# Performance work log

Measured on AMD Instinct MI355X. Metric: run time of the kernel, lower is better.

Reference implementation:

```python
import jax, jax.numpy as jnp
import numpy as np
import math

B, N, C = 16, 4096, 256
WS = 8            # window_size
NH = 8            # num_heads
HD = C // NH      # head_dim = 32
LK = 32           # linformer compressed length
G = 16            # global bank tokens


def setup_inputs() -> dict:
    key = jax.random.key(0)
    ks = jax.random.split(key, 10)
    x = jax.random.normal(ks[0], (B, N, C), dtype=jnp.float32)
    W_qkv = jax.random.normal(ks[1], (C, 3 * C), dtype=jnp.float32) * 0.02
    b_qkv = jnp.zeros((3 * C,), dtype=jnp.float32)
    E_k = jax.random.normal(ks[2], (WS * WS, LK), dtype=jnp.float32) * 0.02
    E_v = jax.random.normal(ks[3], (WS * WS, LK), dtype=jnp.float32) * 0.02
    k_bank = jax.random.normal(ks[4], (G, C), dtype=jnp.float32)
    v_bank = jax.random.normal(ks[5], (G, C), dtype=jnp.float32)
    W_proj = jax.random.normal(ks[6], (C, C), dtype=jnp.float32) * 0.02
    b_proj = jnp.zeros((C,), dtype=jnp.float32)
    return {"x": x, "W_qkv": W_qkv, "b_qkv": b_qkv, "E_k": E_k, "E_v": E_v,
            "k_bank": k_bank, "v_bank": v_bank, "W_proj": W_proj, "b_proj": b_proj,
            "window_size": WS, "num_heads": NH}


def reference(x, W_qkv, b_qkv, E_k, E_v, k_bank, v_bank, W_proj, b_proj, window_size, num_heads):
    Bb, Nn, Cc = x.shape
    Hs = int(math.isqrt(Nn))          # H = W = sqrt(N), divisible by window_size here
    ws = window_size
    nh = Hs // ws                      # windows per side
    hd = Cc // num_heads
    NW = ws * ws                       # tokens per window

    # ---- window partition: [B,N,C] -> [BW, NW, C]
    xw = x.reshape(Bb, nh, ws, nh, ws, Cc).transpose(0, 1, 3, 2, 4, 5)
    xw = xw.reshape(Bb * nh * nh, NW, Cc)
    BW = xw.shape[0]

    # ---- qkv projection and head split: (3, BW, H, NW, hd)
    qkv = (xw @ W_qkv + b_qkv).reshape(BW, NW, 3, num_heads, hd)
    qkv = qkv.transpose(2, 0, 3, 1, 4)
    q, k, v = qkv[0], qkv[1], qkv[2]

    # ---- Linformer KV compression: NW == seq_len (no pad branch)
    k_c = jnp.einsum('nk,bhnd->bhkd', E_k, k)   # [BW,H,LK,hd]
    v_c = jnp.einsum('nk,bhnd->bhkd', E_v, v)

    # ---- global memory bank, broadcast to all windows: [BW,H,G,hd]
    Gt = k_bank.shape[0]
    kb = jnp.broadcast_to(k_bank.reshape(Gt, num_heads, hd).transpose(1, 0, 2)[None],
                          (BW, num_heads, Gt, hd))
    vb = jnp.broadcast_to(v_bank.reshape(Gt, num_heads, hd).transpose(1, 0, 2)[None],
                          (BW, num_heads, Gt, hd))

    k_full = jnp.concatenate([k_c, kb], axis=2)  # [BW,H,LK+G,hd]
    v_full = jnp.concatenate([v_c, vb], axis=2)

    # ---- SDPA (dropout_p = 0)
    scale = 1.0 / math.sqrt(hd)
    scores = jnp.einsum('bhqd,bhkd->bhqk', q, k_full) * scale
    attn = jax.nn.softmax(scores, axis=-1)
    out = jnp.einsum('bhqk,bhkd->bhqd', attn, v_full)     # [BW,H,NW,hd]

    out = out.transpose(0, 2, 1, 3).reshape(BW, NW, Cc)
    out = out @ W_proj + b_proj

    # ---- window reverse: [BW,NW,C] -> [B,N,C]
    out = out.reshape(Bb, nh, nh, ws, ws, Cc).transpose(0, 1, 3, 2, 4, 5)
    out = out.reshape(Bb, Hs * Hs, Cc)
    return out
```

## Files before the change

kernel.cpp:

```cpp
#include <hip/hip_runtime.h>
#include <hip/hip_bf16.h>


typedef unsigned int uint;
typedef __attribute__((ext_vector_type(8))) short short8;
typedef __attribute__((ext_vector_type(4))) float f32x4;
typedef __attribute__((ext_vector_type(4))) uint uintx4;

__device__ __forceinline__ float bup(uint hs) {
    return __uint_as_float(hs << 16);
}
__device__ __forceinline__ uint f2b(float f) {
    __hip_bfloat16 h = __float2bfloat16(f);
    unsigned short u;
    __builtin_memcpy(&u, &h, 2);
    return (uint)u;
}
__device__ __forceinline__ uint f2b2(float a, float b) {
    __hip_bfloat162 h = __float22bfloat162_rn(make_float2(a, b));
    uint u;
    __builtin_memcpy(&u, &h, 4);
    return u;
}
__device__ __forceinline__ f32x4 mfma16(short8 a, short8 b, f32x4 c) {
    return __builtin_amdgcn_mfma_f32_16x16x32_bf16(a, b, c, 0, 0, 0);
}
__device__ __forceinline__ int sw256(int r, int c) { return r * 256 + (c ^ ((r & 7) << 3)); }

__device__ __forceinline__ short8 xpose(f32x4 a, f32x4 b, float s, int lane) {
    const uint pa0 = f2b2(a[0] * s, a[1] * s), pa1 = f2b2(a[2] * s, a[3] * s);
    const uint pb0 = f2b2(b[0] * s, b[1] * s), pb1 = f2b2(b[2] * s, b[3] * s);
    const int s0 = ((lane >> 4) & 1) * 32 + (lane & 15);
    const int s1 = s0 + 16;
    const uint w0a = __shfl(pa0, s0), w0b = __shfl(pb0, s0);
    const uint w1a = __shfl(pa1, s0), w1b = __shfl(pb1, s0);
    const uint w2a = __shfl(pa0, s1), w2b = __shfl(pb0, s1);
    const uint w3a = __shfl(pa1, s1), w3b = __shfl(pb1, s1);
    const bool hi = lane >= 32;
    uintx4 u;
    u[0] = hi ? w0b : w0a;
    u[1] = hi ? w1b : w1a;
    u[2] = hi ? w2b : w2a;
    u[3] = hi ? w3b : w3a;
    short8 r;
    __builtin_memcpy(&r, &u, 16);
    return r;
}
__device__ __forceinline__ short8 xpose_half(f32x4 a, float s, int lane) {
    const uint pa0 = f2b2(a[0] * s, a[1] * s), pa1 = f2b2(a[2] * s, a[3] * s);
    const int s0 = ((lane >> 4) & 1) * 32 + (lane & 15);
    const int s1 = s0 + 16;
    const uint w0a = __shfl(pa0, s0);
    const uint w1a = __shfl(pa1, s0);
    const uint w2a = __shfl(pa0, s1);
    const uint w3a = __shfl(pa1, s1);
    const bool hi = lane >= 32;
    uintx4 u;
    u[0] = hi ? 0u : w0a;
    u[1] = hi ? 0u : w1a;
    u[2] = hi ? 0u : w2a;
    u[3] = hi ? 0u : w3a;
    short8 r;
    __builtin_memcpy(&r, &u, 16);
    return r;
}

#define WS_WHQ 0
#define WS_WHP 196608
#define WS_WLP 262144
#define WS_EKT 327680
#define WS_EVT 329728
#define WS_KBF 331776
#define WS_VBF 335872

__global__ void __launch_bounds__(256)
eswa_prep(const float* __restrict__ Wqkv, const float* __restrict__ Wproj,
          const float* __restrict__ Ek, const float* __restrict__ Ev,
          const float* __restrict__ kbank, const float* __restrict__ vbank,
          short* __restrict__ wsp)
{
    const int blk = blockIdx.x, thr = threadIdx.x;
    if (blk < 192) {
        const int jh = blk & 1;
        const int g = (blk >> 1) * 256 + thr;
        const int lane = g & 63, tk = (g >> 6) & 7, tn = g >> 9;
        const int quad = lane >> 4, l16 = lane & 15;
        const int c = tn * 16 + l16;
        const int r0 = tk * 32 + quad * 8 + jh * 4;
        const float w0 = Wqkv[(r0 + 0) * 768 + c], w1 = Wqkv[(r0 + 1) * 768 + c];
        const float w2 = Wqkv[(r0 + 2) * 768 + c], w3 = Wqkv[(r0 + 3) * 768 + c];
        *(uint2*)(wsp + WS_WHQ + ((tn * 8 + tk) * 64 + lane) * 8 + jh * 4) =
            make_uint2(f2b2(w0, w1), f2b2(w2, w3));
    } else if (blk < 256) {
        const int idx = blk - 192, jh = idx & 1;
        const int g = (idx >> 1) * 256 + thr;
        const int lane = g & 63, tk = (g >> 6) & 7, tn = g >> 9;
        const int quad = lane >> 4, l16 = lane & 15;
        const int c = tn * 16 + l16;
        const int r0 = tk * 32 + quad * 8 + jh * 4;
        float w[4];
        #pragma unroll
        for (int j = 0; j < 4; ++j) w[j] = Wproj[(r0 + j) * 256 + c];
        const uint h01 = f2b2(w[0], w[1]), h23 = f2b2(w[2], w[3]);
        const float l0 = w[0] - bup(h01 & 0xffffu), l1 = w[1] - bup(h01 >> 16);
        const float l2 = w[2] - bup(h23 & 0xffffu), l3 = w[3] - bup(h23 >> 16);
        const int o = ((tn * 8 + tk) * 64 + lane) * 8 + jh * 4;
        *(uint2*)(wsp + WS_WHP + o) = make_uint2(h01, h23);
        *(uint2*)(wsp + WS_WLP + o) = make_uint2(f2b2(l0, l1), f2b2(l2, l3));
    } else if (blk < 258) {
        const float* E = (blk == 256) ? Ek : Ev;
        const int base = (blk == 256) ? WS_EKT : WS_EVT;
        const int lane = thr & 63, tk = (thr >> 6) & 1, tm = (thr >> 7) & 1;
        const int quad = lane >> 4, l16 = lane & 15;
        const int lk = tm * 16 + l16;
        uint pk[4];
        #pragma unroll
        for (int jp = 0; jp < 4; ++jp) {
            const int t = tk * 32 + quad * 8 + jp * 2;
            pk[jp] = f2b2(E[t * 32 + lk], E[(t + 1) * 32 + lk]);
        }
        *(uint4*)(wsp + base + ((tm * 2 + tk) * 64 + lane) * 8) =
            make_uint4(pk[0], pk[1], pk[2], pk[3]);
    } else {
        for (int idx = thr; idx < 512; idx += 256) {
            const int hh = idx >> 6, l = idx & 63;
            const int l16 = l & 15, q = l >> 4;
            uint pk[4];
            #pragma unroll
            for (int jp = 0; jp < 4; ++jp)
                pk[jp] = f2b2(kbank[l16 * 256 + hh * 32 + q * 8 + jp * 2],
                              kbank[l16 * 256 + hh * 32 + q * 8 + jp * 2 + 1]);
            *(uint4*)(wsp + WS_KBF + idx * 8) = make_uint4(pk[0], pk[1], pk[2], pk[3]);
        }
        for (int idx = thr; idx < 1024; idx += 256) {
            const int hh = idx >> 7, md = (idx >> 6) & 1, l = idx & 63;
            const int l16 = l & 15, q = l >> 4;
            uint pk[4] = {0u, 0u, 0u, 0u};
            if (q < 2) {
                #pragma unroll
                for (int jp = 0; jp < 4; ++jp)
                    pk[jp] = f2b2(vbank[(q * 8 + jp * 2) * 256 + hh * 32 + md * 16 + l16],
                                  vbank[(q * 8 + jp * 2 + 1) * 256 + hh * 32 + md * 16 + l16]);
            }
            *(uint4*)(wsp + WS_VBF + idx * 8) = make_uint4(pk[0], pk[1], pk[2], pk[3]);
        }
    }
}

#define SMEM_BYTES 32768

__global__ void __launch_bounds__(512, 3)
eswa_main(const float* __restrict__ x, const float* __restrict__ bqkv,
          const float* __restrict__ bproj, const short* __restrict__ wsp,
          float* __restrict__ out)
{
    extern __shared__ char smem[];
    short* xh   = (short*)smem;
    short* attn = (short*)smem;

    const int tid  = threadIdx.x;
    const int wave = tid >> 6;
    const int lane = tid & 63;
    const int quad = lane >> 4;
    const int l16  = lane & 15;
    const int h    = wave;

    const int b  = blockIdx.x >> 6;
    const int w  = blockIdx.x & 63;
    const int rw = w >> 3;
    const int cw = w & 7;

    #pragma unroll
    for (int i = 0; i < 8; ++i) {
        const int vi = tid + 512 * i;
        const int t  = vi >> 6;
        const int c  = (vi & 63) * 4;
        const int n  = (rw * 8 + (t >> 3)) * 64 + cw * 8 + (t & 7);
        const float4 xv = *(const float4*)(x + (size_t)(b * 4096 + n) * 256 + c);
        *(uint2*)(xh + sw256(t, c)) = make_uint2(f2b2(xv.x, xv.y), f2b2(xv.z, xv.w));
    }
    __syncthreads();

    const short* WF = wsp + WS_WHQ;

    short8 kcf[2], vcf[2];
    {
        f32x4 acc[2][4];
        #pragma unroll
        for (int nd = 0; nd < 2; ++nd) {
            const float bk = bqkv[256 + h * 32 + nd * 16 + l16];
            #pragma unroll
            for (int mt = 0; mt < 4; ++mt) acc[nd][mt] = (f32x4){bk, bk, bk, bk};
        }
        #pragma unroll 2
        for (int tk = 0; tk < 8; ++tk) {
            short8 xf[4];
            #pragma unroll
            for (int mt = 0; mt < 4; ++mt)
                xf[mt] = *(const short8*)(xh + sw256(mt * 16 + l16, tk * 32 + quad * 8));
            #pragma unroll
            for (int nd = 0; nd < 2; ++nd) {
                const short8 wf =
                    *(const short8*)(WF + (((16 + h * 2 + nd) * 8 + tk) * 64 + lane) * 8);
                #pragma unroll
                for (int mt = 0; mt < 4; ++mt) acc[nd][mt] = mfma16(xf[mt], wf, acc[nd][mt]);
            }
        }
        short8 kfr[2][2];
        #pragma unroll
        for (int nd = 0; nd < 2; ++nd)
            #pragma unroll
            for (int kk = 0; kk < 2; ++kk)
                kfr[nd][kk] = xpose(acc[nd][2 * kk], acc[nd][2 * kk + 1], 1.0f, lane);
        short8 ekf[2][2];
        #pragma unroll
        for (int tm = 0; tm < 2; ++tm)
            #pragma unroll
            for (int kk = 0; kk < 2; ++kk)
                ekf[tm][kk] = *(const short8*)(wsp + WS_EKT + ((tm * 2 + kk) * 64 + lane) * 8);
        f32x4 ck[2][2];
        #pragma unroll
        for (int md = 0; md < 2; ++md)
            #pragma unroll
            for (int nl = 0; nl < 2; ++nl) ck[md][nl] = (f32x4){0, 0, 0, 0};
        #pragma unroll
        for (int kk = 0; kk < 2; ++kk)
            #pragma unroll
            for (int md = 0; md < 2; ++md)
                #pragma unroll
                for (int nl = 0; nl < 2; ++nl)
                    ck[md][nl] = mfma16(kfr[md][kk], ekf[nl][kk], ck[md][nl]);
        #pragma unroll
        for (int nl = 0; nl < 2; ++nl)
            kcf[nl] = xpose(ck[0][nl], ck[1][nl], 1.0f, lane);
    }
    {
        f32x4 acc[2][4];
        #pragma unroll
        for (int nd = 0; nd < 2; ++nd) {
            const float bv = bqkv[512 + h * 32 + nd * 16 + l16];
            #pragma unroll
            for (int mt = 0; mt < 4; ++mt) acc[nd][mt] = (f32x4){bv, bv, bv, bv};
        }
        #pragma unroll 2
        for (int tk = 0; tk < 8; ++tk) {
            short8 xf[4];
            #pragma unroll
            for (int mt = 0; mt < 4; ++mt)
                xf[mt] = *(const short8*)(xh + sw256(mt * 16 + l16, tk * 32 + quad * 8));
            #pragma unroll
            for (int nd = 0; nd < 2; ++nd) {
                const short8 wf =
                    *(const short8*)(WF + (((32 + h * 2 + nd) * 8 + tk) * 64 + lane) * 8);
                #pragma unroll
                for (int mt = 0; mt < 4; ++mt) acc[nd][mt] = mfma16(xf[mt], wf, acc[nd][mt]);
            }
        }
        short8 vfr[2][2];
        #pragma unroll
        for (int nd = 0; nd < 2; ++nd)
            #pragma unroll
            for (int kk = 0; kk < 2; ++kk)
                vfr[nd][kk] = xpose(acc[nd][2 * kk], acc[nd][2 * kk + 1], 1.0f, lane);
        short8 evf[2][2];
        #pragma unroll
        for (int tm = 0; tm < 2; ++tm)
            #pragma unroll
            for (int kk = 0; kk < 2; ++kk)
                evf[tm][kk] = *(const short8*)(wsp + WS_EVT + ((tm * 2 + kk) * 64 + lane) * 8);
        f32x4 cv[2][2];
        #pragma unroll
        for (int ml = 0; ml < 2; ++ml)
            #pragma unroll
            for (int nd = 0; nd < 2; ++nd) cv[ml][nd] = (f32x4){0, 0, 0, 0};
        #pragma unroll
        for (int kk = 0; kk < 2; ++kk)
            #pragma unroll
            for (int ml = 0; ml < 2; ++ml)
                #pragma unroll
                for (int nd = 0; nd < 2; ++nd)
                    cv[ml][nd] = mfma16(evf[ml][kk], vfr[nd][kk], cv[ml][nd]);
        #pragma unroll
        for (int nd = 0; nd < 2; ++nd)
            vcf[nd] = xpose(cv[0][nd], cv[1][nd], 1.0f, lane);
    }

    short8 qfr[4];
    {
        f32x4 acc[2][4];
        #pragma unroll
        for (int md = 0; md < 2; ++md) {
            const float4 bq = *(const float4*)(bqkv + h * 32 + md * 16 + quad * 4);
            #pragma unroll
            for (int nt = 0; nt < 4; ++nt) acc[md][nt] = (f32x4){bq.x, bq.y, bq.z, bq.w};
        }
        #pragma unroll 2
        for (int tk = 0; tk < 8; ++tk) {
            short8 xf[4];
            #pragma unroll
            for (int nt = 0; nt < 4; ++nt)
                xf[nt] = *(const short8*)(xh + sw256(nt * 16 + l16, tk * 32 + quad * 8));
            #pragma unroll
            for (int md = 0; md < 2; ++md) {
                const short8 wf =
                    *(const short8*)(WF + (((h * 2 + md) * 8 + tk) * 64 + lane) * 8);
                #pragma unroll
                for (int nt = 0; nt < 4; ++nt) acc[md][nt] = mfma16(wf, xf[nt], acc[md][nt]);
            }
        }
        #pragma unroll
        for (int nt = 0; nt < 4; ++nt)
            qfr[nt] = xpose(acc[0][nt], acc[1][nt], 0.17677669529663687f, lane);
    }
    const short8 kbf = *(const short8*)(wsp + WS_KBF + (h * 64 + lane) * 8);
    short8 vbf[2];
    #pragma unroll
    for (int md = 0; md < 2; ++md)
        vbf[md] = *(const short8*)(wsp + WS_VBF + ((h * 2 + md) * 64 + lane) * 8);
    __syncthreads();

    const f32x4 zero4 = (f32x4){0, 0, 0, 0};
    #pragma unroll
    for (int tt = 0; tt < 4; ++tt) {
        f32x4 sc[3];
        sc[0] = mfma16(kcf[0], qfr[tt], zero4);
        sc[1] = mfma16(kcf[1], qfr[tt], zero4);
        sc[2] = mfma16(kbf,    qfr[tt], zero4);
        float mm = sc[0][0];
        #pragma unroll
        for (int n = 0; n < 3; ++n)
            #pragma unroll
            for (int r = 0; r < 4; ++r) mm = fmaxf(mm, sc[n][r]);
        mm = fmaxf(mm, __shfl_xor(mm, 16));
        mm = fmaxf(mm, __shfl_xor(mm, 32));
        float su = 0.0f;
        #pragma unroll
        for (int n = 0; n < 3; ++n)
            #pragma unroll
            for (int r = 0; r < 4; ++r) {
                const float e = __expf(sc[n][r] - mm);
                sc[n][r] = e;
                su += e;
            }
        su += __shfl_xor(su, 16);
        su += __shfl_xor(su, 32);
        const float inv = 1.0f / su;
        const short8 pa0 = xpose(sc[0], sc[1], inv, lane);
        const short8 pa1 = xpose_half(sc[2], inv, lane);
        #pragma unroll
        for (int md = 0; md < 2; ++md) {
            f32x4 o = mfma16(vcf[md], pa0, zero4);
            o = mfma16(vbf[md], pa1, o);
            *(uint2*)(attn + sw256(tt * 16 + l16, h * 32 + md * 16 + quad * 4)) =
                make_uint2(f2b2(o[0], o[1]), f2b2(o[2], o[3]));
        }
    }
    __syncthreads();

    {
        const short* Whp = wsp + WS_WHP;
        const short* Wlp = wsp + WS_WLP;
        f32x4 acc[2][4];
        #pragma unroll
        for (int p = 0; p < 2; ++p) {
            const float bi = bproj[(wave * 2 + p) * 16 + l16];
            #pragma unroll
            for (int m = 0; m < 4; ++m) acc[p][m] = (f32x4){bi, bi, bi, bi};
        }
        #pragma unroll 2
        for (int tk = 0; tk < 8; ++tk) {
            short8 aA[4];
            #pragma unroll
            for (int m = 0; m < 4; ++m)
                aA[m] = *(const short8*)(attn + sw256(m * 16 + l16, tk * 32 + quad * 8));
            #pragma unroll
            for (int p = 0; p < 2; ++p) {
                const int bo = (((wave * 2 + p) * 8 + tk) * 64 + lane) * 8;
                const short8 bh = *(const short8*)(Whp + bo);
                const short8 bl = *(const short8*)(Wlp + bo);
                #pragma unroll
                for (int m = 0; m < 4; ++m) {
                    acc[p][m] = mfma16(aA[m], bh, acc[p][m]);
                    acc[p][m] = mfma16(aA[m], bl, acc[p][m]);
                }
            }
        }
        #pragma unroll
        for (int p = 0; p < 2; ++p)
            #pragma unroll
            for (int m = 0; m < 4; ++m)
                #pragma unroll
                for (int r = 0; r < 4; ++r) {
                    const int t = m * 16 + quad * 4 + r;
                    const int n = (rw * 8 + (t >> 3)) * 64 + cw * 8 + (t & 7);
                    out[(size_t)(b * 4096 + n) * 256 + (wave * 2 + p) * 16 + l16] =
                        acc[p][m][r];
                }
    }
}

extern "C" void kernel_launch(void* const* d_in, const int* in_sizes, int n_in,
                              void* d_out, int out_size, void* d_ws, size_t ws_size,
                              hipStream_t stream) {
    const float* x     = (const float*)d_in[0];
    const float* Wqkv  = (const float*)d_in[1];
    const float* bqkv  = (const float*)d_in[2];
    const float* Ek    = (const float*)d_in[3];
    const float* Ev    = (const float*)d_in[4];
    const float* kbank = (const float*)d_in[5];
    const float* vbank = (const float*)d_in[6];
    const float* Wproj = (const float*)d_in[7];
    const float* bproj = (const float*)d_in[8];
    float* outp        = (float*)d_out;
    short* wsp         = (short*)d_ws;
    (void)in_sizes; (void)n_in; (void)out_size; (void)ws_size;

    (void)hipFuncSetAttribute((const void*)eswa_main,
                              hipFuncAttributeMaxDynamicSharedMemorySize, SMEM_BYTES);

    eswa_prep<<<259, 256, 0, stream>>>(Wqkv, Wproj, Ek, Ev, kbank, vbank, wsp);
    eswa_main<<<1024, 512, SMEM_BYTES, stream>>>(x, bqkv, bproj, wsp, outp);
}
```

Measured before the change: 176.8 us.

## Shrink live register set in QKV projections to allow six blocks per CU

Raises the launch-bounds minimum blocks per CU from 3 to 6. To make that fit, the K/V projection loops now accumulate one output column tile at a time and reload x fragments from LDS per MFMA, and the Q projection is split into two halves. The hipFuncSetAttribute call is now made only once through a static flag. The goal is more resident waves to hide latency. The cost is extra LDS reads of x, and possible spills if the compiler cannot meet the tighter VGPR budget.

```diff
diff --git a/kernel.cpp b/kernel.cpp
--- a/kernel.cpp
+++ b/kernel.cpp
@@ -149,7 +149,7 @@
 
 #define SMEM_BYTES 32768
 
-__global__ void __launch_bounds__(512, 3)
+__global__ void __launch_bounds__(512, 6)
 eswa_main(const float* __restrict__ x, const float* __restrict__ bqkv,
           const float* __restrict__ bproj, const short* __restrict__ wsp,
           float* __restrict__ out)
@@ -185,139 +185,123 @@
 
     short8 kcf[2], vcf[2];
     {
-        f32x4 acc[2][4];
+        short8 kfr[2][2];
         #pragma unroll
         for (int nd = 0; nd < 2; ++nd) {
+            f32x4 acc[4];
             const float bk = bqkv[256 + h * 32 + nd * 16 + l16];
             #pragma unroll
-            for (int mt = 0; mt < 4; ++mt) acc[nd][mt] = (f32x4){bk, bk, bk, bk};
+            for (int mt = 0; mt < 4; ++mt) acc[mt] = (f32x4){bk, bk, bk, bk};
+            #pragma unroll 2
+            for (int tk = 0; tk < 8; ++tk) {
+                const short8 wf =
+                    *(const short8*)(WF + (((16 + h * 2 + nd) * 8 + tk) * 64 + lane) * 8);
+                #pragma unroll
+                for (int mt = 0; mt < 4; ++mt) {
+                    const short8 xf =
+                        *(const short8*)(xh + sw256(mt * 16 + l16, tk * 32 + quad * 8));
+                    acc[mt] = mfma16(xf, wf, acc[mt]);
+                }
+            }
+            kfr[nd][0] = xpose(acc[0], acc[1], 1.0f, lane);
+            kfr[nd][1] = xpose(acc[2], acc[3], 1.0f, lane);
+        }
+        f32x4 ck[2][2];
+        #pragma unroll
+        for (int md = 0; md < 2; ++md)
+            #pragma unroll
+            for (int nl = 0; nl < 2; ++nl) ck[md][nl] = (f32x4){0, 0, 0, 0};
+        #pragma unroll
+        for (int kk = 0; kk < 2; ++kk)
+            #pragma unroll
+            for (int nl = 0; nl < 2; ++nl) {
+                const short8 ekf =
+                    *(const short8*)(wsp + WS_EKT + ((nl * 2 + kk) * 64 + lane) * 8);
+                #pragma unroll
+                for (int md = 0; md < 2; ++md)
+                    ck[md][nl] = mfma16(kfr[md][kk], ekf, ck[md][nl]);
+            }
+        #pragma unroll
+        for (int nl = 0; nl < 2; ++nl)
+            kcf[nl] = xpose(ck[0][nl], ck[1][nl], 1.0f, lane);
+    }
+    {
+        short8 vfr[2][2];
+        #pragma unroll
+        for (int nd = 0; nd < 2; ++nd) {
+            f32x4 acc[4];
+            const float bv = bqkv[512 + h * 32 + nd * 16 + l16];
+            #pragma unroll
+            for (int mt = 0; mt < 4; ++mt) acc[mt] = (f32x4){bv, bv, bv, bv};
+            #pragma unroll 2
+            for (int tk = 0; tk < 8; ++tk) {
+                const short8 wf =
+                    *(const short8*)(WF + (((32 + h * 2 + nd) * 8 + tk) * 64 + lane) * 8);
+                #pragma unroll
+                for (int mt = 0; mt < 4; ++mt) {
+                    const short8 xf =
+                        *(const short8*)(xh + sw256(mt * 16 + l16, tk * 32 + quad * 8));
+                    acc[mt] = mfma16(xf, wf, acc[mt]);
+                }
+            }
+            vfr[nd][0] = xpose(acc[0], acc[1], 1.0f, lane);
+            vfr[nd][1] = xpose(acc[2], acc[3], 1.0f, lane);
+        }
+        f32x4 cv[2][2];
+        #pragma unroll
+        for (int ml = 0; ml < 2; ++ml)
+            #pragma unroll
+            for (int nd = 0; nd < 2; ++nd) cv[ml][nd] = (f32x4){0, 0, 0, 0};
+        #pragma unroll
+        for (int kk = 0; kk < 2; ++kk)
+            #pragma unroll
+            for (int ml = 0; ml < 2; ++ml) {
+                const short8 evf =
+                    *(const short8*)(wsp + WS_EVT + ((ml * 2 + kk) * 64 + lane) * 8);
+                #pragma unroll
+                for (int nd = 0; nd < 2; ++nd)
+                    cv[ml][nd] = mfma16(evf, vfr[nd][kk], cv[ml][nd]);
+            }
+        #pragma unroll
+        for (int nd = 0; nd < 2; ++nd)
+            vcf[nd] = xpose(cv[0][nd], cv[1][nd], 1.0f, lane);
+    }
+    short8 qfr[4];
+    #pragma unroll
+    for (int hf = 0; hf < 2; ++hf) {
+        f32x4 acc[2][2];
+        #pragma unroll
+        for (int md = 0; md < 2; ++md) {
+            const float4 bq = *(const float4*)(bqkv + h * 32 + md * 16 + quad * 4);
+            #pragma unroll
+            for (int p = 0; p < 2; ++p) acc[md][p] = (f32x4){bq.x, bq.y, bq.z, bq.w};
         }
         #pragma unroll 2
         for (int tk = 0; tk < 8; ++tk) {
-            short8 xf[4];
-            #pragma unroll
-            for (int mt = 0; mt < 4; ++mt)
-                xf[mt] = *(const short8*)(xh + sw256(mt * 16 + l16, tk * 32 + quad * 8));
-            #pragma unroll
-            for (int nd = 0; nd < 2; ++nd) {
-                const short8 wf =
-                    *(const short8*)(WF + (((16 + h * 2 + nd) * 8 + tk) * 64 + lane) * 8);
-                #pragma unroll
-                for (int mt = 0; mt < 4; ++mt) acc[nd][mt] = mfma16(xf[mt], wf, acc[nd][mt]);
-            }
-        }
-        short8 kfr[2][2];
-        #pragma unroll
-        for (int nd = 0; nd < 2; ++nd)
-            #pragma unroll
-            for (int kk = 0; kk < 2; ++kk)
-                kfr[nd][kk] = xpose(acc[nd][2 * kk], acc[nd][2 * kk + 1], 1.0f, lane);
-        short8 ekf[2][2];
-        #pragma unroll
-        for (int tm = 0; tm < 2; ++tm)
-            #pragma unroll
-            for (int kk = 0; kk < 2; ++kk)
-                ekf[tm][kk] = *(const short8*)(wsp + WS_EKT + ((tm * 2 + kk) * 64 + lane) * 8);
-        f32x4 ck[2][2];
-        #pragma unroll
-        for (int md = 0; md < 2; ++md)
-            #pragma unroll
-            for (int nl = 0; nl < 2; ++nl) ck[md][nl] = (f32x4){0, 0, 0, 0};
-        #pragma unroll
-        for (int kk = 0; kk < 2; ++kk)
-            #pragma unroll
-            for (int md = 0; md < 2; ++md)
-                #pragma unroll
-                for (int nl = 0; nl < 2; ++nl)
-                    ck[md][nl] = mfma16(kfr[md][kk], ekf[nl][kk], ck[md][nl]);
-        #pragma unroll
-        for (int nl = 0; nl < 2; ++nl)
-            kcf[nl] = xpose(ck[0][nl], ck[1][nl], 1.0f, lane);
-    }
-    {
-        f32x4 acc[2][4];
-        #pragma unroll
-        for (int nd = 0; nd < 2; ++nd) {
-            const float bv = bqkv[512 + h * 32 + nd * 16 + l16];
-            #pragma unroll
-            for (int mt = 0; mt < 4; ++mt) acc[nd][mt] = (f32x4){bv, bv, bv, bv};
-        }
-        #pragma unroll 2
-        for (int tk = 0; tk < 8; ++tk) {
-            short8 xf[4];
-            #pragma unroll
-            for (int mt = 0; mt < 4; ++mt)
-                xf[mt] = *(const short8*)(xh + sw256(mt * 16 + l16, tk * 32 + quad * 8));
-            #pragma unroll
-            for (int nd = 0; nd < 2; ++nd) {
-                const short8 wf =
-                    *(const short8*)(WF + (((32 + h * 2 + nd) * 8 + tk) * 64 + lane) * 8);
-                #pragma unroll
-                for (int mt = 0; mt < 4; ++mt) acc[nd][mt] = mfma16(xf[mt], wf, acc[nd][mt]);
-            }
-        }
-        short8 vfr[2][2];
-        #pragma unroll
-        for (int nd = 0; nd < 2; ++nd)
-            #pragma unroll
-            for (int kk = 0; kk < 2; ++kk)
-                vfr[nd][kk] = xpose(acc[nd][2 * kk], acc[nd][2 * kk + 1], 1.0f, lane);
-        short8 evf[2][2];
-        #pragma unroll
-        for (int tm = 0; tm < 2; ++tm)
-            #pragma unroll
-            for (int kk = 0; kk < 2; ++kk)
-                evf[tm][kk] = *(const short8*)(wsp + WS_EVT + ((tm * 2 + kk) * 64 + lane) * 8);
-        f32x4 cv[2][2];
-        #pragma unroll
-        for (int ml = 0; ml < 2; ++ml)
-            #pragma unroll
-            for (int nd = 0; nd < 2; ++nd) cv[ml][nd] = (f32x4){0, 0, 0, 0};
-        #pragma unroll
-        for (int kk = 0; kk < 2; ++kk)
-            #pragma unroll
-            for (int ml = 0; ml < 2; ++ml)
-                #pragma unroll
-                for (int nd = 0; nd < 2; ++nd)
-                    cv[ml][nd] = mfma16(evf[ml][kk], vfr[nd][kk], cv[ml][nd]);
-        #pragma unroll
-        for (int nd = 0; nd < 2; ++nd)
-            vcf[nd] = xpose(cv[0][nd], cv[1][nd], 1.0f, lane);
-    }
-
-    short8 qfr[4];
-    {
-        f32x4 acc[2][4];
-        #pragma unroll
-        for (int md = 0; md < 2; ++md) {
-            const float4 bq = *(const float4*)(bqkv + h * 32 + md * 16 + quad * 4);
-            #pragma unroll
-            for (int nt = 0; nt < 4; ++nt) acc[md][nt] = (f32x4){bq.x, bq.y, bq.z, bq.w};
-        }
-        #pragma unroll 2
-        for (int tk = 0; tk < 8; ++tk) {
-            short8 xf[4];
-            #pragma unroll
-            for (int nt = 0; nt < 4; ++nt)
-                xf[nt] = *(const short8*)(xh + sw256(nt * 16 + l16, tk * 32 + quad * 8));
+            short8 xf[2];
+            #pragma unroll
+            for (int p = 0; p < 2; ++p)
+                xf[p] = *(const short8*)(xh + sw256((hf * 2 + p) * 16 + l16,
+                                                    tk * 32 + quad * 8));
             #pragma unroll
             for (int md = 0; md < 2; ++md) {
                 const short8 wf =
                     *(const short8*)(WF + (((h * 2 + md) * 8 + tk) * 64 + lane) * 8);
                 #pragma unroll
-                for (int nt = 0; nt < 4; ++nt) acc[md][nt] = mfma16(wf, xf[nt], acc[md][nt]);
-            }
-        }
-        #pragma unroll
-        for (int nt = 0; nt < 4; ++nt)
-            qfr[nt] = xpose(acc[0][nt], acc[1][nt], 0.17677669529663687f, lane);
-    }
+                for (int p = 0; p < 2; ++p) acc[md][p] = mfma16(wf, xf[p], acc[md][p]);
+            }
+        }
+        #pragma unroll
+        for (int p = 0; p < 2; ++p)
+            qfr[hf * 2 + p] = xpose(acc[0][p], acc[1][p], 0.17677669529663687f, lane);
+    }
+    __syncthreads();
+
     const short8 kbf = *(const short8*)(wsp + WS_KBF + (h * 64 + lane) * 8);
     short8 vbf[2];
     #pragma unroll
     for (int md = 0; md < 2; ++md)
         vbf[md] = *(const short8*)(wsp + WS_VBF + ((h * 2 + md) * 64 + lane) * 8);
-    __syncthreads();
 
     const f32x4 zero4 = (f32x4){0, 0, 0, 0};
     #pragma unroll
@@ -415,8 +399,13 @@
     short* wsp         = (short*)d_ws;
     (void)in_sizes; (void)n_in; (void)out_size; (void)ws_size;
 
-    (void)hipFuncSetAttribute((const void*)eswa_main,
-                              hipFuncAttributeMaxDynamicSharedMemorySize, SMEM_BYTES);
+    static bool attr_set = false;
+    if (!attr_set) {
+        (void)hipFuncSetAttribute((const void*)eswa_main,
+                                  hipFuncAttributeMaxDynamicSharedMemorySize,
+                                  SMEM_BYTES);
+        attr_set = true;
+    }
 
     eswa_prep<<<259, 256, 0, stream>>>(Wqkv, Wproj, Ek, Ev, kbank, vbank, wsp);
     eswa_main<<<1024, 512, SMEM_BYTES, stream>>>(x, bqkv, bproj, wsp, outp);
```

After: 205.7 us. +16.3%, slower.
